# Kernel optimization log

Hardware: AMD Instinct MI355X
Metric: run time of the kernel (lower is better)

## Reference

```python
import jax, jax.numpy as jnp
import numpy as np

B, S, E, H = 4, 2048, 256, 8
DK = E // H


def setup_inputs() -> dict:
    key = jax.random.key(0)
    ks = jax.random.split(key, 12)
    glorot = lambda k, shape: jax.random.uniform(k, shape, jnp.float32, -1.0, 1.0) * jnp.sqrt(6.0 / (shape[0] + shape[1]))
    inp = {
        "q": jax.random.normal(ks[0], (B, S, E), jnp.float32),
        "k": jax.random.normal(ks[1], (B, S, E), jnp.float32),
        "v": jax.random.normal(ks[2], (B, S, E), jnp.float32),
        # causal mask, np.triu(k=1)==0 -> lower triangular including diagonal
        "mask": (jnp.triu(jnp.ones((S, S), jnp.int32), k=1) == 0).astype(jnp.int32)[None, None],
        "Wq": glorot(ks[3], (E, E)), "bq": jnp.zeros((E,), jnp.float32),
        "Wk": glorot(ks[4], (E, E)), "bk": jnp.zeros((E,), jnp.float32),
        "Wv": glorot(ks[5], (E, E)), "bv": jnp.zeros((E,), jnp.float32),
        "Wo": glorot(ks[6], (E, E)), "bo": jnp.zeros((E,), jnp.float32),
        "gammas": glorot(ks[7], (H, 1)).reshape(H, 1, 1),  # xavier init of (H,1,1)
    }
    return inp


def reference(q, k, v, mask, Wq, bq, Wk, bk, Wv, bv, Wo, bo, gammas):
    b, s, e = q.shape
    h = gammas.shape[0]
    dk = e // h
    neg = jnp.float32(-1e32)

    def proj(x, W, bias):
        return (x @ W.T + bias).reshape(b, s, h, dk).transpose(0, 2, 1, 3)  # [B,H,S,dk]

    qh, kh, vh = proj(q, Wq, bq), proj(k, Wk, bk), proj(v, Wv, bv)
    scores = jnp.einsum("bhid,bhjd->bhij", qh, kh) / jnp.sqrt(jnp.float32(dk))  # [B,H,S,S]

    # --- no_grad block: monotonic distance-decay term ---
    maskf = mask.astype(scores.dtype)
    s1 = jax.nn.softmax(jnp.where(mask == 0, neg, scores), axis=-1) * maskf
    s1 = jax.lax.stop_gradient(s1)
    distcum = jnp.cumsum(s1, axis=-1)
    disttotal = jnp.sum(s1, axis=-1, keepdims=True)
    idx = jnp.arange(s)
    pos = jnp.abs(idx[None, :] - idx[:, None]).astype(scores.dtype)[None, None]  # |i-j|
    dist = jnp.sqrt(jnp.clip((disttotal - distcum) * pos, 0.0, None))
    dist = jax.lax.stop_gradient(dist)
    # ----------------------------------------------------

    gamma = -jax.nn.softplus(gammas)[None]                      # [1,H,1,1]
    total_effect = jnp.clip(jnp.exp(dist * gamma), 1e-5, 1e5)
    scores = jnp.where(mask == 0, neg, scores * total_effect)
    attn = jax.nn.softmax(scores, axis=-1)                      # zero_pad=False (mask=1 path)
    out = jnp.einsum("bhij,bhjd->bhid", attn, vh)
    concat = out.transpose(0, 2, 1, 3).reshape(b, s, e)
    return concat @ Wo.T + bo
```

## Files before the change

kernel.cpp:

```cpp
#include <hip/hip_runtime.h>
#include <math.h>

#define B_   4
#define S_   2048
#define E_   256
#define H_   8
#define DK_  32
#define NROWS (B_*S_)

typedef unsigned short ushort_t;
typedef __attribute__((ext_vector_type(8))) short  bf16x8;
typedef __attribute__((ext_vector_type(4))) float  f32x4;

#define LOG2E 1.4426950408889634f
#define QSCALE (0.17677669529663687f * 1.4426950408889634f)

#if __has_builtin(__builtin_amdgcn_exp2f)
#define EXP2F(x) __builtin_amdgcn_exp2f(x)
#else
#define EXP2F(x) exp2f(x)
#endif
#if __has_builtin(__builtin_amdgcn_sqrtf)
#define SQRTF(x) __builtin_amdgcn_sqrtf(x)
#else
#define SQRTF(x) sqrtf(x)
#endif
#if __has_builtin(__builtin_amdgcn_rcpf)
#define RCPF(x) __builtin_amdgcn_rcpf(x)
#else
#define RCPF(x) (1.0f/(x))
#endif

__device__ __forceinline__ ushort_t bf16_rne(float x)
{
    unsigned int u = __float_as_uint(x);
    unsigned int r = u + 0x7FFFu + ((u >> 16) & 1u);
    return (ushort_t)(r >> 16);
}
__device__ __forceinline__ float bf16_to_f(ushort_t h)
{
    return __uint_as_float(((unsigned int)h) << 16);
}

__device__ __forceinline__ float scan16(float x)
{
    x += __int_as_float(__builtin_amdgcn_update_dpp(0, __float_as_int(x), 0x111, 0xF, 0xF, true));
    x += __int_as_float(__builtin_amdgcn_update_dpp(0, __float_as_int(x), 0x112, 0xF, 0xF, true));
    x += __int_as_float(__builtin_amdgcn_update_dpp(0, __float_as_int(x), 0x114, 0xF, 0xF, true));
    x += __int_as_float(__builtin_amdgcn_update_dpp(0, __float_as_int(x), 0x118, 0xF, 0xF, true));
    return x;
}
__device__ __forceinline__ float bcast15(float x)
{
    return __int_as_float(__builtin_amdgcn_ds_swizzle(__float_as_int(x), 0x1F0));
}


__global__ __launch_bounds__(256)
void conv_all(const float* __restrict__ q, const float* __restrict__ k,
              const float* __restrict__ v,
              const float* __restrict__ Wq, const float* __restrict__ Wk,
              const float* __restrict__ Wv, const float* __restrict__ Wo,
              ushort_t* __restrict__ xh, ushort_t* __restrict__ xl,
              ushort_t* __restrict__ wh, ushort_t* __restrict__ wl)
{
    const int z = blockIdx.y;
    const float* src;
    ushort_t *dh, *dl;
    if (z < 3) {
        src = (z == 0) ? q : (z == 1) ? k : v;
        dh = xh + (size_t)z * (NROWS * E_);
        dl = xl + (size_t)z * (NROWS * E_);
    } else {
        if (blockIdx.x >= 16) return;
        src = (z == 3) ? Wq : (z == 4) ? Wk : (z == 5) ? Wv : Wo;
        dh = wh + (size_t)(z - 3) * (E_ * E_);
        dl = wl + (size_t)(z - 3) * (E_ * E_);
    }
    const int n0 = blockIdx.x * 16;
    const int lr = threadIdx.x & 15, kq = threadIdx.x >> 4;
    #pragma unroll
    for (int half = 0; half < 2; half++) {
        const int kk = kq * 8 + half * 128;
        const float* s = src + (size_t)(n0 + lr) * E_ + kk;
        const float4 a = *(const float4*)s;
        const float4 b = *(const float4*)(s + 4);
        const float xs[8] = {a.x, a.y, a.z, a.w, b.x, b.y, b.z, b.w};
        bf16x8 hv, lv;
        #pragma unroll
        for (int e = 0; e < 8; e++) {
            const ushort_t hb = bf16_rne(xs[e]);
            hv[e] = (short)hb;
            lv[e] = (short)bf16_rne(xs[e] - bf16_to_f(hb));
        }
        const size_t o = ((size_t)blockIdx.x * 8 + (kk >> 5)) * 512
                       + ((kk >> 3) & 3) * 128 + lr * 8;
        *(bf16x8*)&dh[o] = hv;
        *(bf16x8*)&dl[o] = lv;
    }
}

__device__ __forceinline__ void gemm_core(
    const ushort_t* __restrict__ Ah, const ushort_t* __restrict__ Al,
    const ushort_t* __restrict__ Bh, const ushort_t* __restrict__ Bl,
    size_t abase, size_t wbase, f32x4 (&acc)[4])
{
    bf16x8 aH = *(const bf16x8*)(Ah + abase);
    bf16x8 aL = *(const bf16x8*)(Al + abase);
    bf16x8 bH[4], bL[4];
    #pragma unroll
    for (int t = 0; t < 4; t++) {
        bH[t] = *(const bf16x8*)(Bh + wbase + (size_t)t * 8 * 512);
        bL[t] = *(const bf16x8*)(Bl + wbase + (size_t)t * 8 * 512);
    }
    #pragma unroll
    for (int kc = 0; kc < 8; kc++) {
        const int kn = (kc + 1) & 7;
        bf16x8 aH2 = *(const bf16x8*)(Ah + abase + (size_t)kn * 512);
        bf16x8 aL2 = *(const bf16x8*)(Al + abase + (size_t)kn * 512);
        bf16x8 bH2[4], bL2[4];
        #pragma unroll
        for (int t = 0; t < 4; t++) {
            bH2[t] = *(const bf16x8*)(Bh + wbase + (size_t)(t * 8 + kn) * 512);
            bL2[t] = *(const bf16x8*)(Bl + wbase + (size_t)(t * 8 + kn) * 512);
        }
        #pragma unroll
        for (int t = 0; t < 4; t++) {
            acc[t] = __builtin_amdgcn_mfma_f32_16x16x32_bf16(aL, bH[t], acc[t], 0, 0, 0);
            acc[t] = __builtin_amdgcn_mfma_f32_16x16x32_bf16(aH, bL[t], acc[t], 0, 0, 0);
            acc[t] = __builtin_amdgcn_mfma_f32_16x16x32_bf16(aH, bH[t], acc[t], 0, 0, 0);
        }
        aH = aH2; aL = aL2;
        #pragma unroll
        for (int t = 0; t < 4; t++) { bH[t] = bH2[t]; bL[t] = bL2[t]; }
    }
}

__global__ __launch_bounds__(256)
void gemm_qkv(const ushort_t* __restrict__ Xh, const ushort_t* __restrict__ Xl,
              const ushort_t* __restrict__ Wh, const ushort_t* __restrict__ Wl,
              const float* __restrict__ bqp, const float* __restrict__ bkp,
              const float* __restrict__ bvp,
              ushort_t* __restrict__ Qh, ushort_t* __restrict__ Ql,
              ushort_t* __restrict__ Kh, ushort_t* __restrict__ Kl,
              ushort_t* __restrict__ Vt)
{
    const size_t N2 = (size_t)NROWS * E_;
    const size_t WN = (size_t)E_ * E_;
    const int z = blockIdx.z;
    const ushort_t* Ah = Xh + (size_t)z * N2;
    const ushort_t* Al = Xl + (size_t)z * N2;
    const ushort_t* Bh = Wh + (size_t)z * WN;
    const ushort_t* Bl = Wl + (size_t)z * WN;
    const float* bias = (z == 0) ? bqp : (z == 1) ? bkp : bvp;
    const float scale = (z == 0) ? QSCALE : 1.0f;

    const int lane = threadIdx.x & 63, wv = threadIdx.x >> 6;
    const int lr = lane & 15, lq = lane >> 4;
    const int mb = blockIdx.x;
    const int nstrip = blockIdx.y * 4 + wv;
    const size_t abase = (size_t)nstrip * 4096 + lane * 8;
    const size_t wbase = (size_t)mb * (4 * 8 * 512) + lane * 8;

    f32x4 acc[4] = {{0,0,0,0},{0,0,0,0},{0,0,0,0},{0,0,0,0}};
    gemm_core(Ah, Al, Bh, Bl, abase, wbase, acc);

    #pragma unroll
    for (int t = 0; t < 4; t++) {
        const int col = mb * 64 + t * 16 + lr;
        const float bt = bias[col];
        const int h = col >> 5, d = col & 31;
        if (z <= 1) {
            ushort_t* Y1 = (z == 0) ? Qh : Kh;
            ushort_t* Y2 = (z == 0) ? Ql : Kl;
            #pragma unroll
            for (int reg = 0; reg < 4; reg++) {
                const int n  = nstrip * 16 + lq * 4 + reg;
                const int bI = n >> 11, sI = n & (S_ - 1);
                const size_t o = (size_t)(bI * H_ + h) * (S_ * DK_)
                               + (size_t)(sI >> 4) * 512
                               + ((d >> 3) & 3) * 128 + (sI & 15) * 8 + (d & 7);
                const float y = (acc[t][reg] + bt) * scale;
                const ushort_t hb = bf16_rne(y);
                Y1[o] = hb;
                Y2[o] = bf16_rne(y - bf16_to_f(hb));
            }
        } else {
            #pragma unroll
            for (int reg = 0; reg < 4; reg++) {
                const int n  = nstrip * 16 + lq * 4 + reg;
                const int bI = n >> 11, sI = n & (S_ - 1);
                const size_t o = (size_t)(bI * H_ + h) * (S_ * DK_)
                               + (size_t)((sI >> 5) * 2 + (d >> 4)) * 512
                               + ((sI >> 3) & 3) * 128 + (d & 15) * 8 + (sI & 7);
                Vt[o] = bf16_rne(acc[t][reg] + bt);
            }
        }
    }
}

__global__ __launch_bounds__(256)
void gemm_out(const ushort_t* __restrict__ Xh, const ushort_t* __restrict__ Xl,
              const ushort_t* __restrict__ Wh, const ushort_t* __restrict__ Wl,
              const float* __restrict__ bias, float* __restrict__ Yf)
{
    const int lane = threadIdx.x & 63, wv = threadIdx.x >> 6;
    const int lr = lane & 15, lq = lane >> 4;
    const int mb = blockIdx.x;
    const int nstrip = blockIdx.y * 4 + wv;
    const size_t abase = (size_t)nstrip * 4096 + lane * 8;
    const size_t wbase = (size_t)mb * (4 * 8 * 512) + lane * 8;

    f32x4 acc[4] = {{0,0,0,0},{0,0,0,0},{0,0,0,0},{0,0,0,0}};
    gemm_core(Xh, Xl, Wh, Wl, abase, wbase, acc);

    #pragma unroll
    for (int t = 0; t < 4; t++) {
        const int col = mb * 64 + t * 16 + lr;
        const float bt = bias[col];
        #pragma unroll
        for (int reg = 0; reg < 4; reg++) {
            const int n = nstrip * 16 + lq * 4 + reg;
            Yf[(size_t)n * E_ + col] = acc[t][reg] + bt;
        }
    }
}

#define VPAD 72

__device__ __forceinline__ void score_tile(f32x4 (&a)[4],
    const ushort_t* __restrict__ Kbh, const ushort_t* __restrict__ Kbl,
    int jt, const bf16x8& qhi, const bf16x8& qlo, int lane, int lr, int lq,
    bool domask, int i0)
{
    #pragma unroll
    for (int tt = 0; tt < 4; tt++) {
        const size_t ko = (size_t)(jt * 4 + tt) * 512 + lane * 8;
        const bf16x8 khi = *(const bf16x8*)(Kbh + ko);
        const bf16x8 klo = *(const bf16x8*)(Kbl + ko);
        f32x4 v = {0.f, 0.f, 0.f, 0.f};
        v = __builtin_amdgcn_mfma_f32_16x16x32_bf16(qlo, khi, v, 0, 0, 0);
        v = __builtin_amdgcn_mfma_f32_16x16x32_bf16(qhi, klo, v, 0, 0, 0);
        v = __builtin_amdgcn_mfma_f32_16x16x32_bf16(qhi, khi, v, 0, 0, 0);
        a[tt] = v;
    }
    if (domask) {
        #pragma unroll
        for (int tt = 0; tt < 4; tt++)
            #pragma unroll
            for (int r = 0; r < 4; r++) {
                const int irow = i0 + lq * 4 + r;
                const int j    = jt * 64 + tt * 16 + lr;
                if (j > irow) a[tt][r] = -3.0e38f;
            }
    }
}

__global__ __launch_bounds__(256)
void attn_flash(const ushort_t* __restrict__ Qh, const ushort_t* __restrict__ Ql,
                const ushort_t* __restrict__ Kh, const ushort_t* __restrict__ Kl,
                const ushort_t* __restrict__ Vs, const float* __restrict__ gammas,
                ushort_t* __restrict__ Ch, ushort_t* __restrict__ Cl)
{
    __shared__ float sTS[16][36];
    __shared__ __align__(16) ushort_t sP[4][16 * VPAD];
    __shared__ float sO[4][16][32];
    __shared__ float sZ[4][16];

    const int tid  = threadIdx.x;
    const int lane = tid & 63, wv = tid >> 6;
    const int lr   = lane & 15, lq = lane >> 4;
    const int unit = blockIdx.x >> 7;
    const int tq   = 31 - unit;
    const int sub  = blockIdx.x & 127;
    const int bh   = sub & 31;
    const int st   = sub >> 5;
    const int h    = bh & 7, b = bh >> 3;
    const int i0   = tq * 64 + st * 16;

    const size_t hb = (size_t)bh * (S_ * DK_);
    const ushort_t* Kbh = Kh + hb;
    const ushort_t* Kbl = Kl + hb;
    const ushort_t* Vb  = Vs + hb;

    const float g   = gammas[h];
    const float gl2 = -((g > 20.f) ? g : log1pf(__expf(g))) * LOG2E;

    const size_t qoff = hb + (size_t)(i0 >> 4) * 512 + lane * 8;
    const bf16x8 qhi = *(const bf16x8*)(Qh + qoff);
    const bf16x8 qlo = *(const bf16x8*)(Ql + qoff);

    for (int jt = wv; jt <= tq; jt += 4) {
        f32x4 a[4];
        score_tile(a, Kbh, Kbl, jt, qhi, qlo, lane, lr, lq, jt == tq, i0);
        #pragma unroll
        for (int r = 0; r < 4; r++) {
            float rs = (EXP2F(a[0][r]) + EXP2F(a[1][r]))
                     + (EXP2F(a[2][r]) + EXP2F(a[3][r]));
            rs += __shfl_xor(rs, 1); rs += __shfl_xor(rs, 2);
            rs += __shfl_xor(rs, 4); rs += __shfl_xor(rs, 8);
            if (lr == 0) sTS[lq * 4 + r][jt] = rs;
        }
    }
    __syncthreads();

    float z2a[4] = {0.f, 0.f, 0.f, 0.f};
    f32x4 O0 = {0.f,0.f,0.f,0.f}, O1 = {0.f,0.f,0.f,0.f};

    if (wv <= tq) {
        float invZ[4], base[4];
        #pragma unroll
        for (int r = 0; r < 4; r++) {
            const int row = lq * 4 + r;
            float run = 0.f, bs = 0.f;
            for (int t = 0; t <= tq; t++) {
                if (t < wv) bs += sTS[row][t];
                run += sTS[row][t];
            }
            invZ[r] = RCPF(run);
            base[r] = bs;
        }

        ushort_t* sPw = &sP[wv][0];
        for (int jt = wv; jt <= tq; jt += 4) {
            const int j0 = jt * 64;
            f32x4 a[4];
            score_tile(a, Kbh, Kbl, jt, qhi, qlo, lane, lr, lq, jt == tq, i0);

            float sc[4][4], tot[4][4];
            #pragma unroll
            for (int tt = 0; tt < 4; tt++)
                #pragma unroll
                for (int r = 0; r < 4; r++) {
                    const float e = EXP2F(a[tt][r]);
                    const float s = scan16(e);
                    sc[tt][r]  = s;
                    tot[tt][r] = bcast15(s);
                }
            #pragma unroll
            for (int r = 0; r < 4; r++) {
                float run2 = base[r];
                #pragma unroll
                for (int tt = 0; tt < 4; tt++) { sc[tt][r] += run2; run2 += tot[tt][r]; }
            }
            #pragma unroll
            for (int tt = 0; tt < 4; tt++) {
                const int j = j0 + tt * 16 + lr;
                #pragma unroll
                for (int r = 0; r < 4; r++) {
                    const int irow = i0 + lq * 4 + r;
                    const float rest = fmaxf(fmaf(-sc[tt][r], invZ[r], 1.0f), 0.f);
                    const float posf = (float)(irow - j);
                    const float dist = SQRTF(fmaxf(rest * posf, 0.f));
                    const float eff  = fmaxf(EXP2F(gl2 * dist), 1e-5f);
                    const float p2   = EXP2F(a[tt][r] * eff);
                    z2a[r] += p2;
                    sPw[(lq * 4 + r) * VPAD + tt * 16 + lr] = bf16_rne(p2);
                }
            }
            #pragma unroll
            for (int kc = 0; kc < 2; kc++) {
                const bf16x8 pa = *(const bf16x8*)&sPw[lr * VPAD + kc * 32 + lq * 8];
                const size_t vb = (size_t)(((j0 >> 5) + kc) * 2) * 512 + lane * 8;
                const bf16x8 v0 = *(const bf16x8*)(Vb + vb);
                const bf16x8 v1 = *(const bf16x8*)(Vb + vb + 512);
                O0 = __builtin_amdgcn_mfma_f32_16x16x32_bf16(pa, v0, O0, 0, 0, 0);
                O1 = __builtin_amdgcn_mfma_f32_16x16x32_bf16(pa, v1, O1, 0, 0, 0);
            }
            if (jt + 4 <= tq) {
                #pragma unroll
                for (int r = 0; r < 4; r++) {
                    const int row = lq * 4 + r;
                    base[r] += sTS[row][jt] + sTS[row][jt+1] + sTS[row][jt+2] + sTS[row][jt+3];
                }
            }
        }
    }

    #pragma unroll
    for (int r = 0; r < 4; r++) {
        float z = z2a[r];
        z += __shfl_xor(z, 1); z += __shfl_xor(z, 2);
        z += __shfl_xor(z, 4); z += __shfl_xor(z, 8);
        if (lr == 0) sZ[wv][lq * 4 + r] = z;
        sO[wv][lq * 4 + r][lr]      = O0[r];
        sO[wv][lq * 4 + r][16 + lr] = O1[r];
    }
    __syncthreads();

    #pragma unroll
    for (int p = 0; p < 2; p++) {
        const int pid = tid + p * 256;
        const int row = pid >> 5, d = pid & 31;
        const float v = (sO[0][row][d] + sO[1][row][d]) + (sO[2][row][d] + sO[3][row][d]);
        const float z = (sZ[0][row] + sZ[1][row]) + (sZ[2][row] + sZ[3][row]);
        const float y = v * RCPF(z);
        const int nIdx = b * S_ + i0 + row;
        const size_t o = ((size_t)(nIdx >> 4) * 8 + h) * 512
                       + (d >> 3) * 128 + (nIdx & 15) * 8 + (d & 7);
        const ushort_t hbb = bf16_rne(y);
        Ch[o] = hbb;
        Cl[o] = bf16_rne(y - bf16_to_f(hbb));
    }
}

extern "C" void kernel_launch(void* const* d_in, const int* in_sizes, int n_in,
                              void* d_out, int out_size, void* d_ws, size_t ws_size,
                              hipStream_t stream)
{
    const float* q      = (const float*)d_in[0];
    const float* k      = (const float*)d_in[1];
    const float* v      = (const float*)d_in[2];
    const float* Wq     = (const float*)d_in[4];
    const float* bq     = (const float*)d_in[5];
    const float* Wk     = (const float*)d_in[6];
    const float* bk     = (const float*)d_in[7];
    const float* Wv     = (const float*)d_in[8];
    const float* bv     = (const float*)d_in[9];
    const float* Wo     = (const float*)d_in[10];
    const float* bo     = (const float*)d_in[11];
    const float* gammas = (const float*)d_in[12];
    float* out = (float*)d_out;

    const size_t N2 = (size_t)NROWS * E_;
    const size_t WN = (size_t)E_ * E_;

    ushort_t* p   = (ushort_t*)d_ws;
    ushort_t* xh  = p;
    ushort_t* xl  = xh + 3 * N2;
    ushort_t* wh  = xl + 3 * N2;
    ushort_t* wl  = wh + 4 * WN;
    ushort_t* qh  = wl + 4 * WN;
    ushort_t* ql  = qh + N2;
    ushort_t* kh  = ql + N2;
    ushort_t* kl  = kh + N2;
    ushort_t* vt  = kl + N2;
    ushort_t* ch  = xh;
    ushort_t* cl  = xh + N2;

    conv_all<<<dim3(NROWS / 16, 7), 256, 0, stream>>>(q, k, v, Wq, Wk, Wv, Wo,
                                                      xh, xl, wh, wl);

    gemm_qkv<<<dim3(E_ / 64, NROWS / 64, 3), 256, 0, stream>>>(
        xh, xl, wh, wl, bq, bk, bv, qh, ql, kh, kl, vt);

    attn_flash<<<32 * 32 * 4, 256, 0, stream>>>(qh, ql, kh, kl, vt, gammas, ch, cl);

    gemm_out<<<dim3(E_ / 64, NROWS / 64), 256, 0, stream>>>(
        ch, cl, wh + 3 * WN, wl + 3 * WN, bo, out);
}
```

Before: 236.2 us.

## Share weight tiles across waves via double-buffered LDS in projection GEMMs

```diff
diff --git a/kernel.cpp b/kernel.cpp
--- a/kernel.cpp
+++ b/kernel.cpp
@@ -100,39 +100,52 @@
     }
 }
 
-__device__ __forceinline__ void gemm_core(
+__device__ __forceinline__ void gemm_lds_core(
     const ushort_t* __restrict__ Ah, const ushort_t* __restrict__ Al,
     const ushort_t* __restrict__ Bh, const ushort_t* __restrict__ Bl,
-    size_t abase, size_t wbase, f32x4 (&acc)[4])
-{
-    bf16x8 aH = *(const bf16x8*)(Ah + abase);
-    bf16x8 aL = *(const bf16x8*)(Al + abase);
-    bf16x8 bH[4], bL[4];
-    #pragma unroll
-    for (int t = 0; t < 4; t++) {
-        bH[t] = *(const bf16x8*)(Bh + wbase + (size_t)t * 8 * 512);
-        bL[t] = *(const bf16x8*)(Bl + wbase + (size_t)t * 8 * 512);
-    }
+    int nstrip, int mb, int wv, int lane,
+    ushort_t* __restrict__ sBh, ushort_t* __restrict__ sBl,
+    f32x4 (&acc)[4])
+{
+    const size_t aoff = (size_t)nstrip * 8 * 512 + lane * 8;
+    const size_t boff = (size_t)(mb * 4 + wv) * 8 * 512 + lane * 8;
+    const int lw = wv * 512 + lane * 8;
+
+    bf16x8 aH = *(const bf16x8*)(Ah + aoff);
+    bf16x8 aL = *(const bf16x8*)(Al + aoff);
+    {
+        const bf16x8 sH = *(const bf16x8*)(Bh + boff);
+        const bf16x8 sL = *(const bf16x8*)(Bl + boff);
+        *(bf16x8*)&sBh[lw] = sH;
+        *(bf16x8*)&sBl[lw] = sL;
+    }
+
     #pragma unroll
     for (int kc = 0; kc < 8; kc++) {
-        const int kn = (kc + 1) & 7;
-        bf16x8 aH2 = *(const bf16x8*)(Ah + abase + (size_t)kn * 512);
-        bf16x8 aL2 = *(const bf16x8*)(Al + abase + (size_t)kn * 512);
-        bf16x8 bH2[4], bL2[4];
+        __syncthreads();
+        const int cur = (kc & 1) * 2048;
+        bf16x8 aH2, aL2, sH2, sL2;
+        if (kc < 7) {
+            aH2 = *(const bf16x8*)(Ah + aoff + (size_t)(kc + 1) * 512);
+            aL2 = *(const bf16x8*)(Al + aoff + (size_t)(kc + 1) * 512);
+            sH2 = *(const bf16x8*)(Bh + boff + (size_t)(kc + 1) * 512);
+            sL2 = *(const bf16x8*)(Bl + boff + (size_t)(kc + 1) * 512);
+        }
         #pragma unroll
         for (int t = 0; t < 4; t++) {
-            bH2[t] = *(const bf16x8*)(Bh + wbase + (size_t)(t * 8 + kn) * 512);
-            bL2[t] = *(const bf16x8*)(Bl + wbase + (size_t)(t * 8 + kn) * 512);
-        }
-        #pragma unroll
-        for (int t = 0; t < 4; t++) {
-            acc[t] = __builtin_amdgcn_mfma_f32_16x16x32_bf16(aL, bH[t], acc[t], 0, 0, 0);
-            acc[t] = __builtin_amdgcn_mfma_f32_16x16x32_bf16(aH, bL[t], acc[t], 0, 0, 0);
-            acc[t] = __builtin_amdgcn_mfma_f32_16x16x32_bf16(aH, bH[t], acc[t], 0, 0, 0);
-        }
-        aH = aH2; aL = aL2;
-        #pragma unroll
-        for (int t = 0; t < 4; t++) { bH[t] = bH2[t]; bL[t] = bL2[t]; }
+            const int ro = cur + t * 512 + lane * 8;
+            const bf16x8 bH = *(const bf16x8*)&sBh[ro];
+            const bf16x8 bL = *(const bf16x8*)&sBl[ro];
+            acc[t] = __builtin_amdgcn_mfma_f32_16x16x32_bf16(aL, bH, acc[t], 0, 0, 0);
+            acc[t] = __builtin_amdgcn_mfma_f32_16x16x32_bf16(aH, bL, acc[t], 0, 0, 0);
+            acc[t] = __builtin_amdgcn_mfma_f32_16x16x32_bf16(aH, bH, acc[t], 0, 0, 0);
+        }
+        if (kc < 7) {
+            const int nx = (cur ^ 2048) + lw;
+            *(bf16x8*)&sBh[nx] = sH2;
+            *(bf16x8*)&sBl[nx] = sL2;
+            aH = aH2; aL = aL2;
+        }
     }
 }
 
@@ -145,6 +158,9 @@
               ushort_t* __restrict__ Kh, ushort_t* __restrict__ Kl,
               ushort_t* __restrict__ Vt)
 {
+    __shared__ __align__(16) ushort_t sBh[2 * 2048];
+    __shared__ __align__(16) ushort_t sBl[2 * 2048];
+
     const size_t N2 = (size_t)NROWS * E_;
     const size_t WN = (size_t)E_ * E_;
     const int z = blockIdx.z;
@@ -159,11 +175,9 @@
     const int lr = lane & 15, lq = lane >> 4;
     const int mb = blockIdx.x;
     const int nstrip = blockIdx.y * 4 + wv;
-    const size_t abase = (size_t)nstrip * 4096 + lane * 8;
-    const size_t wbase = (size_t)mb * (4 * 8 * 512) + lane * 8;
 
     f32x4 acc[4] = {{0,0,0,0},{0,0,0,0},{0,0,0,0},{0,0,0,0}};
-    gemm_core(Ah, Al, Bh, Bl, abase, wbase, acc);
+    gemm_lds_core(Ah, Al, Bh, Bl, nstrip, mb, wv, lane, sBh, sBl, acc);
 
     #pragma unroll
     for (int t = 0; t < 4; t++) {
@@ -204,15 +218,16 @@
               const ushort_t* __restrict__ Wh, const ushort_t* __restrict__ Wl,
               const float* __restrict__ bias, float* __restrict__ Yf)
 {
+    __shared__ __align__(16) ushort_t sBh[2 * 2048];
+    __shared__ __align__(16) ushort_t sBl[2 * 2048];
+
     const int lane = threadIdx.x & 63, wv = threadIdx.x >> 6;
     const int lr = lane & 15, lq = lane >> 4;
     const int mb = blockIdx.x;
     const int nstrip = blockIdx.y * 4 + wv;
-    const size_t abase = (size_t)nstrip * 4096 + lane * 8;
-    const size_t wbase = (size_t)mb * (4 * 8 * 512) + lane * 8;
 
     f32x4 acc[4] = {{0,0,0,0},{0,0,0,0},{0,0,0,0},{0,0,0,0}};
-    gemm_core(Xh, Xl, Wh, Wl, abase, wbase, acc);
+    gemm_lds_core(Xh, Xl, Wh, Wl, nstrip, mb, wv, lane, sBh, sBl, acc);
 
     #pragma unroll
     for (int t = 0; t < 4; t++) {
@@ -308,7 +323,7 @@
     f32x4 O0 = {0.f,0.f,0.f,0.f}, O1 = {0.f,0.f,0.f,0.f};
 
     if (wv <= tq) {
-        float invZ[4], base[4];
+        float invZ[4], base[4], pr[4];
         #pragma unroll
         for (int r = 0; r < 4; r++) {
             const int row = lq * 4 + r;
@@ -319,6 +334,7 @@
             }
             invZ[r] = RCPF(run);
             base[r] = bs;
+            pr[r]   = (float)(i0 + row - lr);
         }
 
         ushort_t* sPw = &sP[wv][0];
@@ -345,14 +361,13 @@
             }
             #pragma unroll
             for (int tt = 0; tt < 4; tt++) {
-                const int j = j0 + tt * 16 + lr;
+                const float jf = (float)(j0 + tt * 16);
                 #pragma unroll
                 for (int r = 0; r < 4; r++) {
-                    const int irow = i0 + lq * 4 + r;
                     const float rest = fmaxf(fmaf(-sc[tt][r], invZ[r], 1.0f), 0.f);
-                    const float posf = (float)(irow - j);
+                    const float posf = pr[r] - jf;
                     const float dist = SQRTF(fmaxf(rest * posf, 0.f));
-                    const float eff  = fmaxf(EXP2F(gl2 * dist), 1e-5f);
+                    const float eff  = EXP2F(gl2 * dist);
                     const float p2   = EXP2F(a[tt][r] * eff);
                     z2a[r] += p2;
                     sPw[(lq * 4 + r) * VPAD + tt * 16 + lr] = bf16_rne(p2);
```

Result: no change. 237.2 us (+0.4%).
